# Kernel tuning notes

Measured on AMD Instinct MI355X. Metric: run time of the kernel, lower is better.

Reference implementation:

```python
import jax, jax.numpy as jnp
import numpy as np

D_MODEL = 1024
NUM_HEADS = 16
D_K = D_MODEL // NUM_HEADS  # 64
MAX_SEQ_LEN = 2048
THETA = 10000.0
BATCH = 2
SEQ = 2048


def _rope_tables():
    # freqs: [d_k/2], positions: [max_seq_len] -> angles [max_seq_len, d_k/2]
    freqs = THETA ** (-jnp.arange(0, D_K, 2, dtype=jnp.float32) / D_K)
    positions = jnp.arange(MAX_SEQ_LEN, dtype=jnp.float32)[:, None]
    angles = positions * freqs[None, :]
    return jnp.cos(angles), jnp.sin(angles)


def _apply_rope(x, token_positions, cos_cached, sin_cached):
    # x: [..., seq, d_k]; token_positions: [seq]
    cos = cos_cached[token_positions]  # [seq, d_k/2]
    sin = sin_cached[token_positions]
    x_even = x[..., ::2]
    x_odd = x[..., 1::2]
    r_even = x_even * cos - x_odd * sin
    r_odd = x_even * sin + x_odd * cos
    # interleave even/odd back into last dim
    out = jnp.stack([r_even, r_odd], axis=-1)
    return out.reshape(x.shape)


def setup_inputs() -> dict:
    key = jax.random.key(0)
    ks = jax.random.split(key, 5)
    scale = 1.0 / np.sqrt(D_MODEL)
    in_features = jax.random.normal(ks[0], (BATCH, SEQ, D_MODEL), dtype=jnp.float32)
    q_proj = jax.random.normal(ks[1], (D_MODEL, D_MODEL), dtype=jnp.float32) * scale
    k_proj = jax.random.normal(ks[2], (D_MODEL, D_MODEL), dtype=jnp.float32) * scale
    v_proj = jax.random.normal(ks[3], (D_MODEL, D_MODEL), dtype=jnp.float32) * scale
    o_proj = jax.random.normal(ks[4], (D_MODEL, D_MODEL), dtype=jnp.float32) * scale
    mask = jnp.tril(jnp.ones((SEQ, SEQ), dtype=bool))  # causal
    token_positions = jnp.arange(SEQ, dtype=jnp.int32)
    return {
        "in_features": in_features,
        "q_proj": q_proj,
        "k_proj": k_proj,
        "v_proj": v_proj,
        "o_proj": o_proj,
        "mask": mask,
        "token_positions": token_positions,
    }


def reference(in_features, q_proj, k_proj, v_proj, o_proj, mask, token_positions):
    B, S, _ = in_features.shape
    cos_cached, sin_cached = _rope_tables()
    # fused QKV projection (same math as x @ cat(Wq,Wk,Wv).T then chunk)
    q = jnp.einsum("bsd,ed->bse", in_features, q_proj)
    k = jnp.einsum("bsd,ed->bse", in_features, k_proj)
    v = jnp.einsum("bsd,ed->bse", in_features, v_proj)
    # ... seq (h d) -> ... h seq d
    q = q.reshape(B, S, NUM_HEADS, D_K).transpose(0, 2, 1, 3)
    k = k.reshape(B, S, NUM_HEADS, D_K).transpose(0, 2, 1, 3)
    v = v.reshape(B, S, NUM_HEADS, D_K).transpose(0, 2, 1, 3)
    q = _apply_rope(q, token_positions, cos_cached, sin_cached)
    k = _apply_rope(k, token_positions, cos_cached, sin_cached)
    scores = jnp.einsum("bhqd,bhkd->bhqk", q, k) / np.sqrt(D_K)
    scores = jnp.where(mask, scores, -jnp.inf)
    attn = jax.nn.softmax(scores, axis=-1)
    out = jnp.einsum("bhqk,bhkd->bhqd", attn, v)
    # ... h seq d -> ... seq (h d)
    concat = out.transpose(0, 2, 1, 3).reshape(B, S, D_MODEL)
    return jnp.einsum("bsd,ed->bse", concat, o_proj)
```

## Files before the change

kernel.cpp:

```cpp
#include <hip/hip_runtime.h>
#include <cstdint>

#define D_MODEL 1024
#define NHEADS 16
#define DKH 64
#define SEQL 2048
#define NBATCH 2
#define NROWS (NBATCH * SEQL)

typedef __bf16 bf16;
typedef __bf16 bf16x2 __attribute__((ext_vector_type(2)));
typedef __bf16 bf16x4 __attribute__((ext_vector_type(4)));
typedef __bf16 bf16x8 __attribute__((ext_vector_type(8)));
typedef float f32x4 __attribute__((ext_vector_type(4)));

static __device__ __forceinline__ f32x4 mfma16(bf16x8 a, bf16x8 b, f32x4 c) {
  return __builtin_amdgcn_mfma_f32_16x16x32_bf16(a, b, c, 0, 0, 0);
}

static __device__ __forceinline__ void gload_lds16(const bf16* g, bf16* l) {
  __builtin_amdgcn_global_load_lds(
      (const __attribute__((address_space(1))) void*)g,
      (__attribute__((address_space(3))) void*)l, 16, 0, 0);
}

static __device__ __forceinline__ float fexp2(float x) {
  return __builtin_amdgcn_exp2f(x);
}

static __device__ __forceinline__ unsigned pack_bf16(float a, float b) {
  unsigned au = __builtin_bit_cast(unsigned, a) + 0x8000u;
  unsigned bu = __builtin_bit_cast(unsigned, b) + 0x8000u;
  return __builtin_amdgcn_perm(bu, au, 0x07060302u);
}

__global__ __launch_bounds__(256) void convert_kernel(
    const float* __restrict__ x, const float* __restrict__ wq,
    const float* __restrict__ wk, const float* __restrict__ wv,
    const float* __restrict__ wo, bf16* __restrict__ xb,
    bf16* __restrict__ wqb, bf16* __restrict__ wkb, bf16* __restrict__ wvb,
    bf16* __restrict__ wob) {
  int i4 = blockIdx.x * 256 + threadIdx.x;
  const float* src;
  bf16* dst;
  int off;
  if (i4 < (NROWS * D_MODEL / 4)) {
    src = x; dst = xb; off = i4;
  } else {
    int j = i4 - NROWS * D_MODEL / 4;
    int sel = j >> 18;
    off = j & ((1 << 18) - 1);
    src = sel == 0 ? wq : sel == 1 ? wk : sel == 2 ? wv : wo;
    dst = sel == 0 ? wqb : sel == 1 ? wkb : sel == 2 ? wvb : wob;
  }
  float4 v = ((const float4*)src)[off];
  bf16x4 o;
  o[0] = (bf16)v.x; o[1] = (bf16)v.y; o[2] = (bf16)v.z; o[3] = (bf16)v.w;
  ((bf16x4*)dst)[off] = o;
}

__global__ __launch_bounds__(256, 3) void qkv_gemm(
    const bf16* __restrict__ A, const bf16* __restrict__ Bq,
    const bf16* __restrict__ Bk, const bf16* __restrict__ Bv,
    const int* __restrict__ tpos, bf16* __restrict__ Qb,
    bf16* __restrict__ Kb, bf16* __restrict__ Vt) {
  __shared__ bf16 As[128 * 64];
  __shared__ bf16 Bs[3][64 * 64];
  const int t = threadIdx.x, wave = t >> 6, lane = t & 63;
  const int quad = lane >> 4, l16 = lane & 15;
  const int bm = blockIdx.x * 128, bn = blockIdx.y * 64;

  f32x4 acc[3][2][4];
  for (int o = 0; o < 3; o++)
    for (int mt = 0; mt < 2; mt++)
      for (int nt = 0; nt < 4; nt++)
        for (int r = 0; r < 4; r++) acc[o][mt][nt][r] = 0.0f;

  for (int k0 = 0; k0 < D_MODEL; k0 += 64) {
    for (int j = 0; j < 4; j++) {
      int s = (wave * 4 + j) * 64 + lane;
      int srow = s >> 3, scol = (s & 7) ^ (srow & 7);
      gload_lds16(&A[(size_t)(bm + srow) * D_MODEL + k0 + scol * 8],
                  &As[(wave * 4 + j) * 512]);
    }
    for (int j = 0; j < 2; j++) {
      int s = (wave * 2 + j) * 64 + lane;
      int srow = s >> 3, scol = (s & 7) ^ (srow & 7);
      size_t goff = (size_t)(bn + srow) * D_MODEL + k0 + scol * 8;
      gload_lds16(&Bq[goff], &Bs[0][(wave * 2 + j) * 512]);
      gload_lds16(&Bk[goff], &Bs[1][(wave * 2 + j) * 512]);
      gload_lds16(&Bv[goff], &Bs[2][(wave * 2 + j) * 512]);
    }
    __syncthreads();
    for (int kh = 0; kh < 2; kh++) {
      const int kc = kh * 4 + quad;
      bf16x8 af[2];
      for (int mt = 0; mt < 2; mt++) {
        int row = wave * 32 + mt * 16 + l16;
        af[mt] = *(bf16x8*)&As[row * 64 + (kc ^ (row & 7)) * 8];
      }
      for (int nt = 0; nt < 4; nt++) {
        int row = nt * 16 + l16;
        int off = row * 64 + (kc ^ (row & 7)) * 8;
        bf16x8 bq = *(bf16x8*)&Bs[0][off];
        bf16x8 bk = *(bf16x8*)&Bs[1][off];
        bf16x8 bv = *(bf16x8*)&Bs[2][off];
        for (int mt = 0; mt < 2; mt++) {
          acc[0][mt][nt] = mfma16(af[mt], bq, acc[0][mt][nt]);
          acc[1][mt][nt] = mfma16(af[mt], bk, acc[1][mt][nt]);
          acc[2][mt][nt] = mfma16(af[mt], bv, acc[2][mt][nt]);
        }
      }
    }
    __syncthreads();
  }

  const float qsc = 0.125f * 1.44269504f;
  float freqv[4], sgn[4];
  for (int nt = 0; nt < 4; nt++) {
    int cp = (bn + nt * 16 + l16) & 63;
    freqv[nt] = fexp2((float)(cp >> 1) * -0.41524101f);
    sgn[nt] = (cp & 1) ? 1.0f : -1.0f;
  }
  for (int mt = 0; mt < 2; mt++) {
    int row0 = bm + wave * 32 + mt * 16 + quad * 4;
    for (int r = 0; r < 4; r++) {
      int row = row0 + r;
      float pos = (float)tpos[row & (SEQL - 1)];
      for (int nt = 0; nt < 4; nt++) {
        int col = bn + nt * 16 + l16;
        float sn, cs;
        __sincosf(pos * freqv[nt], &sn, &cs);
        float vq = acc[0][mt][nt][r];
        float vk = acc[1][mt][nt][r];
        float pq = __shfl_xor(vq, 1);
        float pk = __shfl_xor(vk, 1);
        float rq = vq * cs + sgn[nt] * pq * sn;
        float rk = vk * cs + sgn[nt] * pk * sn;
        Qb[(size_t)row * D_MODEL + col] = (bf16)(rq * qsc);
        Kb[(size_t)row * D_MODEL + col] = (bf16)rk;
      }
    }
    for (int nt = 0; nt < 4; nt++) {
      int col = bn + nt * 16 + l16;
      bf16x4 pv;
      for (int r = 0; r < 4; r++) pv[r] = (bf16)acc[2][mt][nt][r];
      *(bf16x4*)&Vt[(size_t)col * NROWS + row0] = pv;
    }
  }
}

template <int BM, int BN, typename OutT>
__device__ __forceinline__ void gemm_body64(const bf16* __restrict__ A,
                                            const bf16* __restrict__ Bm,
                                            OutT* __restrict__ C, int bm,
                                            int bn, int N, int K) {
  constexpr int MT = BM / 32, NT = BN / 32;
  constexpr int CA = BM / 32, CB = BN / 32;
  __shared__ bf16 As[BM * 64];
  __shared__ bf16 Bs[BN * 64];
  const int t = threadIdx.x;
  const int wave = t >> 6, lane = t & 63;
  const int quad = lane >> 4, l16 = lane & 15;
  const int wm = (wave >> 1) * (MT * 16), wn = (wave & 1) * (NT * 16);

  f32x4 acc[MT][NT];
  for (int i = 0; i < MT; i++)
    for (int j = 0; j < NT; j++)
      for (int r = 0; r < 4; r++) acc[i][j][r] = 0.0f;

  for (int k0 = 0; k0 < K; k0 += 64) {
    for (int j = 0; j < CA; j++) {
      int s = (wave * CA + j) * 64 + lane;
      int srow = s >> 3, scol = (s & 7) ^ (srow & 7);
      gload_lds16(&A[(size_t)(bm + srow) * K + k0 + scol * 8],
                  &As[(wave * CA + j) * 512]);
    }
    for (int j = 0; j < CB; j++) {
      int s = (wave * CB + j) * 64 + lane;
      int srow = s >> 3, scol = (s & 7) ^ (srow & 7);
      gload_lds16(&Bm[(size_t)(bn + srow) * K + k0 + scol * 8],
                  &Bs[(wave * CB + j) * 512]);
    }
    __syncthreads();
    for (int kh = 0; kh < 2; kh++) {
      const int kc = kh * 4 + quad;
      bf16x8 af[MT], bfr[NT];
      for (int mt = 0; mt < MT; mt++) {
        int row = wm + mt * 16 + l16;
        af[mt] = *(bf16x8*)&As[row * 64 + (kc ^ (row & 7)) * 8];
      }
      for (int nt = 0; nt < NT; nt++) {
        int row = wn + nt * 16 + l16;
        bfr[nt] = *(bf16x8*)&Bs[row * 64 + (kc ^ (row & 7)) * 8];
      }
      for (int mt = 0; mt < MT; mt++)
        for (int nt = 0; nt < NT; nt++)
          acc[mt][nt] = mfma16(af[mt], bfr[nt], acc[mt][nt]);
    }
    __syncthreads();
  }
  for (int mt = 0; mt < MT; mt++)
    for (int nt = 0; nt < NT; nt++)
      for (int r = 0; r < 4; r++) {
        int row = bm + wm + mt * 16 + quad * 4 + r;
        int col = bn + wn + nt * 16 + l16;
        C[(size_t)row * N + col] = (OutT)acc[mt][nt][r];
      }
}

__global__ __launch_bounds__(256, 3) void o_gemm(const bf16* __restrict__ A,
                                                 const bf16* __restrict__ Bm,
                                                 float* __restrict__ C) {
  gemm_body64<64, 128, float>(A, Bm, C, blockIdx.x * 64, blockIdx.y * 128,
                              D_MODEL, D_MODEL);
}

__global__ __launch_bounds__(256) void attn_kernel(
    const bf16* __restrict__ Q, const bf16* __restrict__ K,
    const bf16* __restrict__ Vt_g, float* __restrict__ O0,
    float* __restrict__ O1, float* __restrict__ O2, float* __restrict__ O3,
    float* __restrict__ L0, float* __restrict__ L1, float* __restrict__ L2,
    float* __restrict__ L3) {
  const int t = threadIdx.x;
  const int wave = t >> 6, lane = t & 63;
  const int quad = lane >> 4, l16 = lane & 15;

  const int id = blockIdx.x;
  const int bh = id & 31;
  const int c = 39 - (id >> 5);
  int qt, piece, np;
  if (c < 4)       { qt = c;                 piece = 0;            np = 1; }
  else if (c < 12) { int e = c - 4;  qt = 4 + (e >> 1); piece = e & 1; np = 2; }
  else if (c < 24) { int e = c - 12; qt = 8 + e / 3;    piece = e % 3; np = 3; }
  else             { int e = c - 24; qt = 12 + (e >> 2); piece = e & 3; np = 4; }
  const int total = qt + 1, bas = total / np, rem = total % np;
  const int len = bas + (piece < rem ? 1 : 0);
  const int k0 = piece * bas + (piece < rem ? piece : rem);
  const int k1 = k0 + len - 1;

  const int b = bh >> 4, h = bh & 15;
  const int q_base = qt * 128;
  const size_t base = (size_t)b * SEQL * D_MODEL + h * DKH;

  __shared__ bf16 Ks[128 * 64];
  __shared__ bf16 Vts[64 * 128];
  __shared__ bf16 Pw[4 * 32 * 32];

  const int r8 = lane >> 3, c8 = lane & 7;
  const int r16 = lane >> 4, c16 = lane & 15;

  for (int i = 0; i < 4; i++) {
    int row = wave * 32 + i * 8 + r8;
    int sc = c8 ^ (row & 7);
    gload_lds16(&Q[base + (size_t)(q_base + row) * D_MODEL + sc * 8],
                &Ks[(wave * 32 + i * 8) * 64]);
  }
  __syncthreads();
  bf16x8 qb[2][2];
  for (int n = 0; n < 2; n++) {
    int row = wave * 32 + n * 16 + l16;
    qb[n][0] = *(bf16x8*)&Ks[row * 64 + (quad ^ (row & 7)) * 8];
    qb[n][1] = *(bf16x8*)&Ks[row * 64 + ((4 + quad) ^ (row & 7)) * 8];
  }
  __syncthreads();

  bf16x8 ones;
  for (int j = 0; j < 8; j++) ones[j] = (bf16)1.0f;
  const f32x4 fz = {0.0f, 0.0f, 0.0f, 0.0f};

  f32x4 oaccT[2][4];
  f32x4 lacc[2];
  for (int n = 0; n < 2; n++) {
    for (int r = 0; r < 4; r++) lacc[n][r] = 0.0f;
    for (int dt = 0; dt < 4; dt++)
      for (int r = 0; r < 4; r++) oaccT[n][dt][r] = 0.0f;
  }

  bf16* P = &Pw[wave * 32 * 32];
  const bf16* Vrow0 = &Vt_g[(size_t)(h * 64) * NROWS + b * SEQL];
  const int px = (l16 >> 1) & 3;

  for (int kv = k0; kv <= k1; kv++) {
    const int kv_base = kv * 128;
    for (int i = 0; i < 4; i++) {
      int row = wave * 32 + i * 8 + r8;
      int sc = c8 ^ (row & 7);
      gload_lds16(&K[base + (size_t)(kv_base + row) * D_MODEL + sc * 8],
                  &Ks[(wave * 32 + i * 8) * 64]);
    }
    for (int i = 0; i < 4; i++) {
      int d = wave * 16 + i * 4 + r16;
      int sc = c16 ^ (d & 7);
      gload_lds16(&Vrow0[(size_t)d * NROWS + kv_base + sc * 8],
                  &Vts[(wave * 16 + i * 4) * 128]);
    }
    __syncthreads();

    const bool diag = (kv == qt);
    for (int cc = 0; cc < 4; cc++) {
      f32x4 sT[2][2];
      for (int m2 = 0; m2 < 2; m2++) {
        int krow = cc * 32 + m2 * 16 + l16;
        bf16x8 kf0 = *(bf16x8*)&Ks[krow * 64 + (quad ^ (krow & 7)) * 8];
        bf16x8 kf1 = *(bf16x8*)&Ks[krow * 64 + ((4 + quad) ^ (krow & 7)) * 8];
        for (int n = 0; n < 2; n++) {
          sT[n][m2] = mfma16(kf0, qb[n][0], fz);
          sT[n][m2] = mfma16(kf1, qb[n][1], sT[n][m2]);
        }
      }
      if (diag) {
        for (int n = 0; n < 2; n++) {
          int q_loc = wave * 32 + n * 16 + l16;
          for (int m2 = 0; m2 < 2; m2++) {
            int key0 = cc * 32 + m2 * 16 + quad * 4;
            for (int r = 0; r < 4; r++)
              if (key0 + r > q_loc) sT[n][m2][r] = -1e30f;
          }
        }
      }
      for (int n = 0; n < 2; n++) {
        int q = n * 16 + l16;
        for (int m2 = 0; m2 < 2; m2++) {
          uint2 u;
          u.x = pack_bf16(fexp2(sT[n][m2][0]), fexp2(sT[n][m2][1]));
          u.y = pack_bf16(fexp2(sT[n][m2][2]), fexp2(sT[n][m2][3]));
          int kc = m2 * 2 + (quad >> 1);
          *(uint2*)&P[q * 32 + ((kc ^ px) * 8) + (quad & 1) * 4] = u;
        }
      }
      bf16x8 pf[2];
      for (int n = 0; n < 2; n++) {
        int q = n * 16 + l16;
        pf[n] = *(bf16x8*)&P[q * 32 + ((quad ^ px) * 8)];
      }
      for (int n = 0; n < 2; n++) lacc[n] = mfma16(ones, pf[n], lacc[n]);
      for (int dt = 0; dt < 4; dt++) {
        int d = dt * 16 + l16;
        bf16x8 vf = *(bf16x8*)&Vts[d * 128 + (((cc * 4 + quad) ^ (d & 7)) * 8)];
        for (int n = 0; n < 2; n++)
          oaccT[n][dt] = mfma16(vf, pf[n], oaccT[n][dt]);
      }
    }
    __syncthreads();
  }

  float* Ob;
  float* Lb;
  int rbase, roff;
  if (piece == 0)      { Ob = O0; Lb = L0; rbase = SEQL;        roff = 0; }
  else if (piece == 1) { Ob = O1; Lb = L1; rbase = SEQL - 512;  roff = 512; }
  else if (piece == 2) { Ob = O2; Lb = L2; rbase = SEQL - 1024; roff = 1024; }
  else                 { Ob = O3; Lb = L3; rbase = SEQL - 1536; roff = 1536; }
  for (int n = 0; n < 2; n++) {
    int qrow = q_base + wave * 32 + n * 16 + l16;
    size_t orow = (size_t)b * rbase + (qrow - roff);
    if (quad == 0) Lb[orow * NHEADS + h] = lacc[n][0];
    for (int dt = 0; dt < 4; dt++)
      *(f32x4*)&Ob[orow * D_MODEL + h * DKH + dt * 16 + quad * 4] =
          oaccT[n][dt];
  }
}

__global__ __launch_bounds__(256) void normalize_kernel(
    const float* __restrict__ O0, const float* __restrict__ O1,
    const float* __restrict__ O2, const float* __restrict__ O3,
    const float* __restrict__ L0, const float* __restrict__ L1,
    const float* __restrict__ L2, const float* __restrict__ L3,
    bf16* __restrict__ Cc) {
  int i4 = blockIdx.x * 256 + threadIdx.x;
  int row = i4 >> 8;
  int c0 = (i4 & 255) * 4;
  int s = row & (SEQL - 1);
  int b = row >> 11;
  int h = c0 >> 6;
  float l = L0[(size_t)row * NHEADS + h];
  f32x4 v = *(const f32x4*)&O0[(size_t)row * D_MODEL + c0];
  if (s >= 512) {
    size_t r1 = (size_t)b * (SEQL - 512) + (s - 512);
    l += L1[r1 * NHEADS + h];
    f32x4 u = *(const f32x4*)&O1[r1 * D_MODEL + c0];
    for (int r = 0; r < 4; r++) v[r] += u[r];
  }
  if (s >= 1024) {
    size_t r2 = (size_t)b * (SEQL - 1024) + (s - 1024);
    l += L2[r2 * NHEADS + h];
    f32x4 u = *(const f32x4*)&O2[r2 * D_MODEL + c0];
    for (int r = 0; r < 4; r++) v[r] += u[r];
  }
  if (s >= 1536) {
    size_t r3 = (size_t)b * (SEQL - 1536) + (s - 1536);
    l += L3[r3 * NHEADS + h];
    f32x4 u = *(const f32x4*)&O3[r3 * D_MODEL + c0];
    for (int r = 0; r < 4; r++) v[r] += u[r];
  }
  float inv = 1.0f / l;
  bf16x4 o;
  o[0] = (bf16)(v[0] * inv);
  o[1] = (bf16)(v[1] * inv);
  o[2] = (bf16)(v[2] * inv);
  o[3] = (bf16)(v[3] * inv);
  *(bf16x4*)&Cc[(size_t)row * D_MODEL + c0] = o;
}

extern "C" void kernel_launch(void* const* d_in, const int* in_sizes, int n_in,
                              void* d_out, int out_size, void* d_ws,
                              size_t ws_size, hipStream_t stream) {
  const float* x = (const float*)d_in[0];
  const float* wq = (const float*)d_in[1];
  const float* wk = (const float*)d_in[2];
  const float* wv = (const float*)d_in[3];
  const float* wo = (const float*)d_in[4];
  const int* tpos = (const int*)d_in[6];
  float* out = (float*)d_out;

  char* p = (char*)d_ws;
  bf16* xb  = (bf16*)p; p += (size_t)NROWS * D_MODEL * 2;
  bf16* wqb = (bf16*)p; p += (size_t)D_MODEL * D_MODEL * 2;
  bf16* wkb = (bf16*)p; p += (size_t)D_MODEL * D_MODEL * 2;
  bf16* wvb = (bf16*)p; p += (size_t)D_MODEL * D_MODEL * 2;
  bf16* wob = (bf16*)p; p += (size_t)D_MODEL * D_MODEL * 2;
  bf16* Qb  = (bf16*)p; p += (size_t)NROWS * D_MODEL * 2;
  bf16* Kb  = (bf16*)p; p += (size_t)NROWS * D_MODEL * 2;
  bf16* Vt  = (bf16*)p; p += (size_t)NROWS * D_MODEL * 2;
  bf16* Cc  = (bf16*)p; p += (size_t)NROWS * D_MODEL * 2;
  float* O0 = (float*)p; p += (size_t)NROWS * D_MODEL * 4;
  float* L0 = (float*)p; p += (size_t)NROWS * NHEADS * 4;
  float* O1 = (float*)p; p += (size_t)NBATCH * (SEQL - 512) * D_MODEL * 4;
  float* L1 = (float*)p; p += (size_t)NBATCH * (SEQL - 512) * NHEADS * 4;
  float* O2 = (float*)xb;
  float* O3 = (float*)wqb;
  float* L2 = (float*)wvb;
  float* L3 = (float*)wvb + (size_t)NBATCH * (SEQL - 1024) * NHEADS;

  convert_kernel<<<8192, 256, 0, stream>>>(x, wq, wk, wv, wo, xb, wqb, wkb,
                                           wvb, wob);
  qkv_gemm<<<dim3(NROWS / 128, D_MODEL / 64), 256, 0, stream>>>(
      xb, wqb, wkb, wvb, tpos, Qb, Kb, Vt);
  attn_kernel<<<1280, 256, 0, stream>>>(Qb, Kb, Vt, O0, O1, O2, O3, L0, L1,
                                        L2, L3);
  normalize_kernel<<<NROWS * D_MODEL / 1024, 256, 0, stream>>>(
      O0, O1, O2, O3, L0, L1, L2, L3, Cc);
  o_gemm<<<dim3(NROWS / 64, D_MODEL / 128), 256, 0, stream>>>(Cc, wob, out);
}
```

Measured before the change: 182.7 us.

## Switch attention to 32x32 MFMA and keep P in registers via permlane swap

Rewrites the attention inner loop to use 32x32x16 bf16 MFMA tiles instead of 16x16x32. The score-to-P transform now uses hardware packed bf16 conversion and v_permlane32_swap, so P stays in registers and no longer goes through the LDS scratch buffer. The row sum is accumulated with scalar adds rather than an MFMA against a ones vector. This removes LDS round trips and extra MFMAs, but changes the accumulator layout and raises register pressure per wave.

Measured after the change: 183.9 us. Within noise of the previous version (+0.7%).

```diff
diff --git a/kernel.cpp b/kernel.cpp
--- a/kernel.cpp
+++ b/kernel.cpp
@@ -13,9 +13,15 @@
 typedef __bf16 bf16x4 __attribute__((ext_vector_type(4)));
 typedef __bf16 bf16x8 __attribute__((ext_vector_type(8)));
 typedef float f32x4 __attribute__((ext_vector_type(4)));
+typedef float f32x16 __attribute__((ext_vector_type(16)));
+typedef unsigned u32x4 __attribute__((ext_vector_type(4)));
 
 static __device__ __forceinline__ f32x4 mfma16(bf16x8 a, bf16x8 b, f32x4 c) {
   return __builtin_amdgcn_mfma_f32_16x16x32_bf16(a, b, c, 0, 0, 0);
+}
+
+static __device__ __forceinline__ f32x16 mfma32(bf16x8 a, bf16x8 b, f32x16 c) {
+  return __builtin_amdgcn_mfma_f32_32x32x16_bf16(a, b, c, 0, 0, 0);
 }
 
 static __device__ __forceinline__ void gload_lds16(const bf16* g, bf16* l) {
@@ -28,10 +34,14 @@
   return __builtin_amdgcn_exp2f(x);
 }
 
-static __device__ __forceinline__ unsigned pack_bf16(float a, float b) {
-  unsigned au = __builtin_bit_cast(unsigned, a) + 0x8000u;
-  unsigned bu = __builtin_bit_cast(unsigned, b) + 0x8000u;
-  return __builtin_amdgcn_perm(bu, au, 0x07060302u);
+static __device__ __forceinline__ unsigned cvt_pk(float a, float b) {
+  unsigned r;
+  asm("v_cvt_pk_bf16_f32 %0, %1, %2" : "=v"(r) : "v"(a), "v"(b));
+  return r;
+}
+
+static __device__ __forceinline__ void plswap(unsigned& a, unsigned& b) {
+  asm("v_permlane32_swap_b32 %0, %1" : "+v"(a), "+v"(b));
 }
 
 __global__ __launch_bounds__(256) void convert_kernel(
@@ -224,7 +234,7 @@
     float* __restrict__ L3) {
   const int t = threadIdx.x;
   const int wave = t >> 6, lane = t & 63;
-  const int quad = lane >> 4, l16 = lane & 15;
+  const int l32 = lane & 31, hi = lane >> 5;
 
   const int id = blockIdx.x;
   const int bh = id & 31;
@@ -245,7 +255,6 @@
 
   __shared__ bf16 Ks[128 * 64];
   __shared__ bf16 Vts[64 * 128];
-  __shared__ bf16 Pw[4 * 32 * 32];
 
   const int r8 = lane >> 3, c8 = lane & 7;
   const int r16 = lane >> 4, c16 = lane & 15;
@@ -257,29 +266,25 @@
                 &Ks[(wave * 32 + i * 8) * 64]);
   }
   __syncthreads();
-  bf16x8 qb[2][2];
-  for (int n = 0; n < 2; n++) {
-    int row = wave * 32 + n * 16 + l16;
-    qb[n][0] = *(bf16x8*)&Ks[row * 64 + (quad ^ (row & 7)) * 8];
-    qb[n][1] = *(bf16x8*)&Ks[row * 64 + ((4 + quad) ^ (row & 7)) * 8];
+  bf16x8 qb[4];
+  {
+    int row = wave * 32 + l32;
+#pragma unroll
+    for (int ks = 0; ks < 4; ks++) {
+      int ch = (ks * 2 + hi) ^ (row & 7);
+      qb[ks] = *(bf16x8*)&Ks[row * 64 + ch * 8];
+    }
   }
   __syncthreads();
 
-  bf16x8 ones;
-  for (int j = 0; j < 8; j++) ones[j] = (bf16)1.0f;
-  const f32x4 fz = {0.0f, 0.0f, 0.0f, 0.0f};
-
-  f32x4 oaccT[2][4];
-  f32x4 lacc[2];
-  for (int n = 0; n < 2; n++) {
-    for (int r = 0; r < 4; r++) lacc[n][r] = 0.0f;
-    for (int dt = 0; dt < 4; dt++)
-      for (int r = 0; r < 4; r++) oaccT[n][dt][r] = 0.0f;
-  }
-
-  bf16* P = &Pw[wave * 32 * 32];
+  f32x16 oaccT[2];
+  float lsum = 0.0f;
+#pragma unroll
+  for (int dt = 0; dt < 2; dt++)
+#pragma unroll
+    for (int r = 0; r < 16; r++) oaccT[dt][r] = 0.0f;
+
   const bf16* Vrow0 = &Vt_g[(size_t)(h * 64) * NROWS + b * SEQL];
-  const int px = (l16 >> 1) & 3;
 
   for (int kv = k0; kv <= k1; kv++) {
     const int kv_base = kv * 128;
@@ -298,53 +303,64 @@
     __syncthreads();
 
     const bool diag = (kv == qt);
+#pragma unroll
     for (int cc = 0; cc < 4; cc++) {
-      f32x4 sT[2][2];
-      for (int m2 = 0; m2 < 2; m2++) {
-        int krow = cc * 32 + m2 * 16 + l16;
-        bf16x8 kf0 = *(bf16x8*)&Ks[krow * 64 + (quad ^ (krow & 7)) * 8];
-        bf16x8 kf1 = *(bf16x8*)&Ks[krow * 64 + ((4 + quad) ^ (krow & 7)) * 8];
-        for (int n = 0; n < 2; n++) {
-          sT[n][m2] = mfma16(kf0, qb[n][0], fz);
-          sT[n][m2] = mfma16(kf1, qb[n][1], sT[n][m2]);
+      f32x16 sT;
+#pragma unroll
+      for (int r = 0; r < 16; r++) sT[r] = 0.0f;
+      {
+        int krow = cc * 32 + l32;
+#pragma unroll
+        for (int ks = 0; ks < 4; ks++) {
+          int ch = (ks * 2 + hi) ^ (krow & 7);
+          bf16x8 kf = *(bf16x8*)&Ks[krow * 64 + ch * 8];
+          sT = mfma32(kf, qb[ks], sT);
         }
       }
       if (diag) {
-        for (int n = 0; n < 2; n++) {
-          int q_loc = wave * 32 + n * 16 + l16;
-          for (int m2 = 0; m2 < 2; m2++) {
-            int key0 = cc * 32 + m2 * 16 + quad * 4;
-            for (int r = 0; r < 4; r++)
-              if (key0 + r > q_loc) sT[n][m2][r] = -1e30f;
-          }
+        int q_loc = wave * 32 + l32;
+#pragma unroll
+        for (int r = 0; r < 16; r++) {
+          int key = cc * 32 + (r & 3) + 8 * (r >> 2) + 4 * hi;
+          if (key > q_loc) sT[r] = -1e30f;
         }
       }
-      for (int n = 0; n < 2; n++) {
-        int q = n * 16 + l16;
-        for (int m2 = 0; m2 < 2; m2++) {
-          uint2 u;
-          u.x = pack_bf16(fexp2(sT[n][m2][0]), fexp2(sT[n][m2][1]));
-          u.y = pack_bf16(fexp2(sT[n][m2][2]), fexp2(sT[n][m2][3]));
-          int kc = m2 * 2 + (quad >> 1);
-          *(uint2*)&P[q * 32 + ((kc ^ px) * 8) + (quad & 1) * 4] = u;
+      float p[16];
+#pragma unroll
+      for (int r = 0; r < 16; r++) p[r] = fexp2(sT[r]);
+      lsum += (((p[0] + p[1]) + (p[2] + p[3])) +
+               ((p[4] + p[5]) + (p[6] + p[7]))) +
+              (((p[8] + p[9]) + (p[10] + p[11])) +
+               ((p[12] + p[13]) + (p[14] + p[15])));
+      unsigned a0 = cvt_pk(p[0], p[1]),  a1 = cvt_pk(p[2], p[3]);
+      unsigned b0 = cvt_pk(p[4], p[5]),  b1 = cvt_pk(p[6], p[7]);
+      unsigned c0 = cvt_pk(p[8], p[9]),  c1 = cvt_pk(p[10], p[11]);
+      unsigned d0 = cvt_pk(p[12], p[13]), d1 = cvt_pk(p[14], p[15]);
+      plswap(a0, b0); plswap(a1, b1); plswap(c0, d0); plswap(c1, d1);
+      bf16x8 pf[2];
+      {
+        u32x4 u = {a0, a1, b0, b1};
+        pf[0] = __builtin_bit_cast(bf16x8, u);
+      }
+      {
+        u32x4 u = {c0, c1, d0, d1};
+        pf[1] = __builtin_bit_cast(bf16x8, u);
+      }
+#pragma unroll
+      for (int dt = 0; dt < 2; dt++) {
+        int d = dt * 32 + l32;
+#pragma unroll
+        for (int ks = 0; ks < 2; ks++) {
+          int ch = (cc * 4 + ks * 2 + hi) ^ (d & 7);
+          bf16x8 vf = *(bf16x8*)&Vts[d * 128 + ch * 8];
+          oaccT[dt] = mfma32(vf, pf[ks], oaccT[dt]);
         }
       }
-      bf16x8 pf[2];
-      for (int n = 0; n < 2; n++) {
-        int q = n * 16 + l16;
-        pf[n] = *(bf16x8*)&P[q * 32 + ((quad ^ px) * 8)];
-      }
-      for (int n = 0; n < 2; n++) lacc[n] = mfma16(ones, pf[n], lacc[n]);
-      for (int dt = 0; dt < 4; dt++) {
-        int d = dt * 16 + l16;
-        bf16x8 vf = *(bf16x8*)&Vts[d * 128 + (((cc * 4 + quad) ^ (d & 7)) * 8)];
-        for (int n = 0; n < 2; n++)
-          oaccT[n][dt] = mfma16(vf, pf[n], oaccT[n][dt]);
-      }
-    }
-    __syncthreads();
-  }
-
+    }
+    __syncthreads();
+  }
+
+  lsum += __shfl_xor(lsum, 32);
   float* Ob;
   float* Lb;
   int rbase, roff;
@@ -352,13 +368,19 @@
   else if (piece == 1) { Ob = O1; Lb = L1; rbase = SEQL - 512;  roff = 512; }
   else if (piece == 2) { Ob = O2; Lb = L2; rbase = SEQL - 1024; roff = 1024; }
   else                 { Ob = O3; Lb = L3; rbase = SEQL - 1536; roff = 1536; }
-  for (int n = 0; n < 2; n++) {
-    int qrow = q_base + wave * 32 + n * 16 + l16;
+  {
+    int qrow = q_base + wave * 32 + l32;
     size_t orow = (size_t)b * rbase + (qrow - roff);
-    if (quad == 0) Lb[orow * NHEADS + h] = lacc[n][0];
-    for (int dt = 0; dt < 4; dt++)
-      *(f32x4*)&Ob[orow * D_MODEL + h * DKH + dt * 16 + quad * 4] =
-          oaccT[n][dt];
+    if (hi == 0) Lb[orow * NHEADS + h] = lsum;
+#pragma unroll
+    for (int dt = 0; dt < 2; dt++)
+#pragma unroll
+      for (int rq = 0; rq < 4; rq++) {
+        f32x4 vv = {oaccT[dt][rq * 4 + 0], oaccT[dt][rq * 4 + 1],
+                    oaccT[dt][rq * 4 + 2], oaccT[dt][rq * 4 + 3]};
+        *(f32x4*)&Ob[orow * D_MODEL + h * DKH + dt * 32 + rq * 8 + hi * 4] =
+            vv;
+      }
   }
 }
 
```
